# Optimization experiments

Hardware: AMD Instinct MI355X
Metric: run time of the kernel (lower is better)

The kernel has to match this reference:

```python
import jax, jax.numpy as jnp
import numpy as np

B = 32768          # batch size (positions)
PIECES = 32        # max active features per position
NNZ = B * PIECES
FT_OUT = 512
NFEAT = 768        # 64 squares * 6 piece types * 2 colors


def setup_inputs() -> dict:
    key = jax.random.key(0)
    k1, k2, k3, k4, k5, k6 = jax.random.split(key, 6)
    rows = jnp.repeat(jnp.arange(B, dtype=jnp.int64), PIECES)  # batch index per nnz
    stm_cols = jax.random.randint(k1, (NNZ,), 0, NFEAT, dtype=jnp.int64)
    nstm_cols = jax.random.randint(k2, (NNZ,), 0, NFEAT, dtype=jnp.int64)
    stm_indices = jnp.stack([rows, stm_cols], axis=0)   # [2, NNZ]
    nstm_indices = jnp.stack([rows, nstm_cols], axis=0)  # [2, NNZ]
    values = jnp.ones((NNZ,), dtype=jnp.float32)
    ft_w = jax.random.normal(k3, (FT_OUT, NFEAT), dtype=jnp.float32) * 0.05
    ft_b = jax.random.normal(k4, (FT_OUT,), dtype=jnp.float32) * 0.05
    out_w = jax.random.normal(k5, (1, 2 * FT_OUT), dtype=jnp.float32) * 0.05
    out_b = jax.random.normal(k6, (1,), dtype=jnp.float32) * 0.05
    return {
        "stm_indices": stm_indices,
        "nstm_indices": nstm_indices,
        "values": values,
        "size": B,
        "ft_w": ft_w,
        "ft_b": ft_b,
        "out_w": out_w,
        "out_b": out_b,
    }


def reference(stm_indices, nstm_indices, values, size, ft_w, ft_b, out_w, out_b):
    # sparse_coo_tensor(...).to_dense(): scatter-add values into dense [size, 768]
    board_stm = jnp.zeros((size, NFEAT), dtype=values.dtype).at[
        stm_indices[0], stm_indices[1]].add(values)
    board_nstm = jnp.zeros((size, NFEAT), dtype=values.dtype).at[
        nstm_indices[0], nstm_indices[1]].add(values)
    # shared feature transformer Linear(768, ft_out)
    stm_ft = board_stm @ ft_w.T + ft_b    # [B, FT_OUT]
    nstm_ft = board_nstm @ ft_w.T + ft_b  # [B, FT_OUT]
    hidden = jnp.clip(jnp.concatenate([stm_ft, nstm_ft], axis=1), 0.0, 1.0)
    return jax.nn.sigmoid(hidden @ out_w.T + out_b)  # [B, 1]
```

## Files before the change

kernel.cpp:

```cpp
#include <hip/hip_runtime.h>

#define BATCH  32768
#define PIECES 32
#define NNZ    (BATCH * PIECES)
#define FT_OUT 512
#define NFEAT  768
#define WSCALE 400.0f

#define POS_PER_BLOCK 32
#define NTHREADS 512
#define NBLOCKS (BATCH / POS_PER_BLOCK)
#define ROW_PITCH 784
#define SIDE_BYTES (POS_PER_BLOCK * ROW_PITCH)
#define PACC_OFF (2 * SIDE_BYTES)
#define LDS_TOTAL (PACC_OFF + 128)

typedef int v4i  __attribute__((ext_vector_type(4)));
typedef int v16i __attribute__((ext_vector_type(16)));

__global__ __launch_bounds__(256) void pack_w_i8(
    const float* __restrict__ ft_w, unsigned char* __restrict__ bpk)
{
    int gid = blockIdx.x * 256 + threadIdx.x;
    int t   = gid / 1536;
    int rem = gid - t * 1536;
    int s   = rem >> 6;
    int l   = rem & 63;
    int g   = l >> 5, ln = l & 31;
    int n   = t * 32 + ln;
    const float* src = ft_w + n * NFEAT + s * 32 + g * 16;
    unsigned ud[4];
    #pragma unroll
    for (int d = 0; d < 4; ++d) {
        unsigned u = 0;
        #pragma unroll
        for (int b = 0; b < 4; ++b) {
            float q = rintf(src[4 * d + b] * WSCALE);
            q = fminf(fmaxf(q, -127.0f), 127.0f);
            u |= ((unsigned)(int)q & 0xffu) << (8 * b);
        }
        ud[d] = u;
    }
    *(uint4*)(bpk + gid * 16) = make_uint4(ud[0], ud[1], ud[2], ud[3]);
}

__global__ __launch_bounds__(NTHREADS, 4) void nn_mfma(
    const int*   __restrict__ stm_idx,
    const int*   __restrict__ nstm_idx,
    const float* __restrict__ values,
    const unsigned char* __restrict__ bpk,
    const float* __restrict__ ft_b,
    const float* __restrict__ out_w,
    const float* __restrict__ out_b,
    float*       __restrict__ out)
{
    extern __shared__ __align__(16) unsigned char lds[];
    unsigned* ldsw = (unsigned*)lds;
    float*    pacc = (float*)(lds + PACC_OFF);

    const int tid  = threadIdx.x;
    const int pos0 = blockIdx.x * POS_PER_BLOCK;

    int colv[4], vqv[4];
    #pragma unroll
    for (int it = 0; it < 4; ++it) {
        int i    = tid + it * NTHREADS;
        int side = i >> 10;
        int r    = i & 1023;
        int nnz  = pos0 * PIECES + r;
        colv[it] = side ? nstm_idx[NNZ + nnz] : stm_idx[NNZ + nnz];
        vqv[it]  = (int)rintf(values[nnz]);
    }

    for (int i = tid; i < LDS_TOTAL / 16; i += NTHREADS)
        ((uint4*)lds)[i] = make_uint4(0u, 0u, 0u, 0u);
    __syncthreads();

    #pragma unroll
    for (int it = 0; it < 4; ++it) {
        int i    = tid + it * NTHREADS;
        int side = i >> 10;
        int pos  = (i & 1023) >> 5;
        int dw   = (side * SIDE_BYTES + pos * ROW_PITCH) >> 2;
        atomicAdd(&ldsw[dw + (colv[it] >> 2)],
                  (unsigned)vqv[it] << (8 * (colv[it] & 3)));
    }
    __syncthreads();

    const int lane = tid & 63, wv = tid >> 6;
    const int ln = lane & 31, g = lane >> 5;
    const float inv_s = 1.0f / WSCALE;

    v16i acc[2][2];
    #pragma unroll
    for (int q = 0; q < 2; ++q)
        #pragma unroll
        for (int sd = 0; sd < 2; ++sd)
            #pragma unroll
            for (int e = 0; e < 16; ++e) acc[q][sd][e] = 0;

    const unsigned char* a0p = lds + ln * ROW_PITCH + g * 16;
    const unsigned char* a1p = a0p + SIDE_BYTES;
    const unsigned char* bp0 = bpk + ((wv * 2 + 0) * 24) * 1024 + lane * 16;
    const unsigned char* bp1 = bpk + ((wv * 2 + 1) * 24) * 1024 + lane * 16;

    uint4 aw0 = *(const uint4*)(a0p);
    uint4 aw1 = *(const uint4*)(a1p);
    uint4 bw0 = *(const uint4*)(bp0);
    uint4 bw1 = *(const uint4*)(bp1);
    #pragma unroll
    for (int ks = 0; ks < 24; ++ks) {
        uint4 na0, na1, nb0, nb1;
        if (ks < 23) {
            na0 = *(const uint4*)(a0p + (ks + 1) * 32);
            na1 = *(const uint4*)(a1p + (ks + 1) * 32);
            nb0 = *(const uint4*)(bp0 + (ks + 1) * 1024);
            nb1 = *(const uint4*)(bp1 + (ks + 1) * 1024);
        }
        v4i af0 = __builtin_bit_cast(v4i, aw0);
        v4i af1 = __builtin_bit_cast(v4i, aw1);
        v4i bf0 = __builtin_bit_cast(v4i, bw0);
        v4i bf1 = __builtin_bit_cast(v4i, bw1);
        acc[0][0] = __builtin_amdgcn_mfma_i32_32x32x32_i8(af0, bf0, acc[0][0], 0, 0, 0);
        acc[0][1] = __builtin_amdgcn_mfma_i32_32x32x32_i8(af1, bf0, acc[0][1], 0, 0, 0);
        acc[1][0] = __builtin_amdgcn_mfma_i32_32x32x32_i8(af0, bf1, acc[1][0], 0, 0, 0);
        acc[1][1] = __builtin_amdgcn_mfma_i32_32x32x32_i8(af1, bf1, acc[1][1], 0, 0, 0);
        aw0 = na0; aw1 = na1; bw0 = nb0; bw1 = nb1;
    }

    float pp[16];
    #pragma unroll
    for (int r = 0; r < 16; ++r) pp[r] = 0.f;

    #pragma unroll
    for (int q = 0; q < 2; ++q) {
        int   n    = (wv * 2 + q) * 32 + ln;
        float bias = ft_b[n];
        float ow0  = out_w[n];
        float ow1  = out_w[FT_OUT + n];
        #pragma unroll
        for (int r = 0; r < 16; ++r) {
            float h0 = fminf(fmaxf((float)acc[q][0][r] * inv_s + bias, 0.f), 1.f);
            float h1 = fminf(fmaxf((float)acc[q][1][r] * inv_s + bias, 0.f), 1.f);
            pp[r] += h0 * ow0 + h1 * ow1;
        }
    }

    #pragma unroll
    for (int r = 0; r < 16; ++r) {
        float v = pp[r];
        v += __shfl_xor(v, 16, 64);
        v += __shfl_xor(v,  8, 64);
        v += __shfl_xor(v,  4, 64);
        v += __shfl_xor(v,  2, 64);
        v += __shfl_xor(v,  1, 64);
        if (ln == 0) {
            int m = (r & 3) + 8 * (r >> 2) + 4 * g;
            atomicAdd(&pacc[m], v);
        }
    }
    __syncthreads();

    if (tid < POS_PER_BLOCK) {
        float p = pacc[tid] + out_b[0];
        out[pos0 + tid] = 1.0f / (1.0f + expf(-p));
    }
}

extern "C" void kernel_launch(void* const* d_in, const int* in_sizes, int n_in,
                              void* d_out, int out_size, void* d_ws, size_t ws_size,
                              hipStream_t stream)
{
    const int*   stm    = (const int*)  d_in[0];
    const int*   nstm   = (const int*)  d_in[1];
    const float* values = (const float*)d_in[2];
    const float* ft_w   = (const float*)d_in[4];
    const float* ft_b   = (const float*)d_in[5];
    const float* out_w  = (const float*)d_in[6];
    const float* out_b  = (const float*)d_in[7];

    unsigned char* bpk = (unsigned char*)d_ws;

    (void)hipFuncSetAttribute((const void*)nn_mfma,
                              hipFuncAttributeMaxDynamicSharedMemorySize,
                              LDS_TOTAL);

    pack_w_i8<<<dim3(96), dim3(256), 0, stream>>>(ft_w, bpk);
    nn_mfma<<<dim3(NBLOCKS), dim3(NTHREADS), LDS_TOTAL, stream>>>(
        stm, nstm, values, bpk, ft_b, out_w, out_b, (float*)d_out);
}
```

Before: 107.3 us.

## Replace shuffle-reduction epilogue with LDS transpose reduction and simplify MFMA loop

The epilogue no longer does 80 cross-lane shuffles per thread plus per-wave atomics. Each thread now writes its partial sums into a padded LDS scratch area that reuses the feature-board space, then all threads sum columns cooperatively before a smaller set of LDS atomics. The MFMA loop also drops its manual register double-buffering in favour of direct loads with partial unroll, leaving scheduling to the compiler. This adds an extra barrier and may expose load latency in the main loop.

```diff
diff --git a/kernel.cpp b/kernel.cpp
--- a/kernel.cpp
+++ b/kernel.cpp
@@ -14,6 +14,7 @@
 #define SIDE_BYTES (POS_PER_BLOCK * ROW_PITCH)
 #define PACC_OFF (2 * SIDE_BYTES)
 #define LDS_TOTAL (PACC_OFF + 128)
+#define SC_PITCH 33
 
 typedef int v4i  __attribute__((ext_vector_type(4)));
 typedef int v16i __attribute__((ext_vector_type(16)));
@@ -56,6 +57,7 @@
 {
     extern __shared__ __align__(16) unsigned char lds[];
     unsigned* ldsw = (unsigned*)lds;
+    float*    scf  = (float*)lds;
     float*    pacc = (float*)(lds + PACC_OFF);
 
     const int tid  = threadIdx.x;
@@ -104,19 +106,12 @@
     const unsigned char* bp0 = bpk + ((wv * 2 + 0) * 24) * 1024 + lane * 16;
     const unsigned char* bp1 = bpk + ((wv * 2 + 1) * 24) * 1024 + lane * 16;
 
-    uint4 aw0 = *(const uint4*)(a0p);
-    uint4 aw1 = *(const uint4*)(a1p);
-    uint4 bw0 = *(const uint4*)(bp0);
-    uint4 bw1 = *(const uint4*)(bp1);
-    #pragma unroll
+    #pragma unroll 4
     for (int ks = 0; ks < 24; ++ks) {
-        uint4 na0, na1, nb0, nb1;
-        if (ks < 23) {
-            na0 = *(const uint4*)(a0p + (ks + 1) * 32);
-            na1 = *(const uint4*)(a1p + (ks + 1) * 32);
-            nb0 = *(const uint4*)(bp0 + (ks + 1) * 1024);
-            nb1 = *(const uint4*)(bp1 + (ks + 1) * 1024);
-        }
+        uint4 aw0 = *(const uint4*)(a0p + ks * 32);
+        uint4 aw1 = *(const uint4*)(a1p + ks * 32);
+        uint4 bw0 = *(const uint4*)(bp0 + ks * 1024);
+        uint4 bw1 = *(const uint4*)(bp1 + ks * 1024);
         v4i af0 = __builtin_bit_cast(v4i, aw0);
         v4i af1 = __builtin_bit_cast(v4i, aw1);
         v4i bf0 = __builtin_bit_cast(v4i, bw0);
@@ -125,7 +120,6 @@
         acc[0][1] = __builtin_amdgcn_mfma_i32_32x32x32_i8(af1, bf0, acc[0][1], 0, 0, 0);
         acc[1][0] = __builtin_amdgcn_mfma_i32_32x32x32_i8(af0, bf1, acc[1][0], 0, 0, 0);
         acc[1][1] = __builtin_amdgcn_mfma_i32_32x32x32_i8(af1, bf1, acc[1][1], 0, 0, 0);
-        aw0 = na0; aw1 = na1; bw0 = nb0; bw1 = nb1;
     }
 
     float pp[16];
@@ -146,18 +140,26 @@
         }
     }
 
-    #pragma unroll
-    for (int r = 0; r < 16; ++r) {
-        float v = pp[r];
-        v += __shfl_xor(v, 16, 64);
-        v += __shfl_xor(v,  8, 64);
-        v += __shfl_xor(v,  4, 64);
-        v += __shfl_xor(v,  2, 64);
-        v += __shfl_xor(v,  1, 64);
-        if (ln == 0) {
+    __syncthreads();
+    {
+        int base = wv * (32 * SC_PITCH) + ln * SC_PITCH;
+        #pragma unroll
+        for (int r = 0; r < 16; ++r) {
             int m = (r & 3) + 8 * (r >> 2) + 4 * g;
-            atomicAdd(&pacc[m], v);
+            scf[base + m] = pp[r];
         }
+    }
+    __syncthreads();
+    {
+        int m = tid & 31, j = tid >> 5;
+        float s = 0.f;
+        #pragma unroll
+        for (int i = 0; i < 16; ++i) {
+            int p   = i * 16 + j;
+            int wvp = p >> 5, lnp = p & 31;
+            s += scf[wvp * (32 * SC_PITCH) + lnp * SC_PITCH + m];
+        }
+        atomicAdd(&pacc[m], s);
     }
     __syncthreads();
 
```

Result: faster. 105.1 us, median of 2 (-2.1%).
